# Optimization experiments

Measured on AMD Instinct MI355X. Metric: run time of the kernel, lower is better.

Reference implementation:

```python
import jax, jax.numpy as jnp
import numpy as np

N_OPS = 8  # eset_ops_3_to_3: identity, 3 single-axis sums, 3 pair sums, full sum (broadcast back)


def _conv(x, w, b):
    # x: (N,C,H,W), w: (O,C,kh,kw), VALID conv, stride 1
    y = jax.lax.conv_general_dilated(x, w, (1, 1), 'VALID',
                                     dimension_numbers=('NCHW', 'OIHW', 'NCHW'))
    return y + b[None, :, None, None]


def _maxpool2(x):
    return jax.lax.reduce_window(x, -jnp.inf, jax.lax.max,
                                 (1, 1, 2, 2), (1, 1, 2, 2), 'VALID')


def _eq3to3(x, W, b):
    # x: (B,i,j,k,d) channels-last; W: (N_OPS,d,o); b: (o,)
    # Fused form: contract each summed basis op with its weight BEFORE broadcasting.
    si = x.sum(1)          # (B,j,k,d)
    sj = x.sum(2)          # (B,i,k,d)
    sk = x.sum(3)          # (B,i,j,d)
    sij = x.sum((1, 2))    # (B,k,d)
    sik = x.sum((1, 3))    # (B,j,d)
    sjk = x.sum((2, 3))    # (B,i,d)
    s = x.sum((1, 2, 3))   # (B,d)
    y = jnp.einsum('bijkd,do->bijko', x, W[0])
    y = y + jnp.einsum('bjkd,do->bjko', si, W[1])[:, None]
    y = y + jnp.einsum('bikd,do->biko', sj, W[2])[:, :, None]
    y = y + jnp.einsum('bijd,do->bijo', sk, W[3])[:, :, :, None]
    y = y + jnp.einsum('bkd,do->bko', sij, W[4])[:, None, None]
    y = y + jnp.einsum('bjd,do->bjo', sik, W[5])[:, None, :, None]
    y = y + jnp.einsum('bid,do->bio', sjk, W[6])[:, :, None, None]
    y = y + jnp.einsum('bd,do->bo', s, W[7])[:, None, None, None]
    return y + b


def setup_inputs() -> dict:
    key = jax.random.key(0)
    ks = jax.random.split(key, 14)
    B, k, h, w = 16, 40, 28, 28
    hid, out_dim = 64, 32
    flat = 64 * 4 * 4  # after conv5-pool2-conv5-pool2 on 28x28
    p = lambda ki, shape, fan: jax.random.normal(ki, shape, jnp.float32) / np.sqrt(fan)
    return {
        'x': jax.random.normal(ks[0], (B, k, h, w), jnp.float32),
        'conv1_w': p(ks[1], (32, 1, 5, 5), 25),
        'conv1_b': jnp.zeros((32,), jnp.float32),
        'conv2_w': p(ks[2], (64, 32, 5, 5), 32 * 25),
        'conv2_b': jnp.zeros((64,), jnp.float32),
        'fc_w': p(ks[3], (flat, hid), flat),
        'fc_b': jnp.zeros((hid,), jnp.float32),
        'eq1_w': p(ks[4], (N_OPS, hid, hid), N_OPS * hid) * 0.1,
        'eq1_b': jnp.zeros((hid,), jnp.float32),
        'eq2_w': p(ks[5], (N_OPS, hid, out_dim), N_OPS * hid) * 0.1,
        'eq2_b': jnp.zeros((out_dim,), jnp.float32),
        'out_w': p(ks[6], (out_dim, 1), out_dim),
        'out_b': jnp.zeros((1,), jnp.float32),
    }


def reference(x, conv1_w, conv1_b, conv2_w, conv2_b, fc_w, fc_b,
              eq1_w, eq1_b, eq2_w, eq2_b, out_w, out_b):
    B, k, h, w = x.shape
    z = x.reshape(B * k, 1, h, w)
    z = _maxpool2(jax.nn.relu(_conv(z, conv1_w, conv1_b)))
    z = _maxpool2(jax.nn.relu(_conv(z, conv2_w, conv2_b)))
    z = z.reshape(B * k, -1) @ fc_w + fc_b
    e = jax.nn.relu(z).reshape(B, k, -1)          # (B,k,d)
    t = jnp.einsum('bid,bjd,bkd->bijkd', e, e, e)  # (B,k,k,k,d) cubic tensor
    y = jax.nn.relu(_eq3to3(t, eq1_w, eq1_b))
    y = _eq3to3(y, eq2_w, eq2_b)                   # (B,k,k,k,out_dim)
    y = jax.nn.relu(y).sum(axis=(1, 2, 3))         # (B,out_dim); dropout_prob=0 (eval)
    y = jax.nn.relu(y)
    return y @ out_w + out_b                       # (B,1)
```

## Files before the change

kernel.cpp:

```cpp
#include <hip/hip_runtime.h>
#include <hip/hip_bf16.h>


typedef unsigned short u16;
typedef __attribute__((ext_vector_type(8))) short bf8_t;
typedef __attribute__((ext_vector_type(4))) float f4_t;

#define LSTR 72

__device__ inline u16 f2bf(float f){
  union { float f; unsigned u; } v; v.f = f;
  unsigned r = v.u + 0x7fffu + ((v.u >> 16) & 1u);
  return (u16)(r >> 16);
}
__device__ inline float bflo(unsigned u){ union { unsigned x; float f; } v; v.x = u << 16; return v.f; }
__device__ inline float bfhi(unsigned u){ union { unsigned x; float f; } v; v.x = u & 0xffff0000u; return v.f; }
__device__ inline unsigned pack2(float a, float b){ return (unsigned)f2bf(a) | ((unsigned)f2bf(b) << 16); }
__device__ inline unsigned permpack(float lo, float hi){
  union { float f; unsigned u; } x, y; x.f = lo; y.f = hi;
  return __builtin_amdgcn_perm(y.u, x.u, 0x07060302u);
}
__device__ inline void unpack8(bf8_t x, float* o){
  union { bf8_t v; unsigned u[4]; } q; q.v = x;
  #pragma unroll
  for (int p = 0; p < 4; ++p){ o[2*p] = bflo(q.u[p]); o[2*p+1] = bfhi(q.u[p]); }
}

__global__ __launch_bounds__(256) void kwp(const float* __restrict__ w2, const float* __restrict__ fcw,
                                           u16* __restrict__ wt2, u16* __restrict__ fcwT){
  int tid = blockIdx.x*256 + threadIdx.x, stride = gridDim.x*256;
  for (int i = tid; i < 51200; i += stride){
    int tap = i >> 11, rc = i & 2047, co = rc >> 5, ci = rc & 31;
    wt2[i] = f2bf(w2[co*800 + ci*25 + tap]);
  }
  for (int i = tid; i < 65536; i += stride){
    int o = i >> 10, k = i & 1023;
    fcwT[i] = f2bf(fcw[k*64 + o]);
  }
}

__global__ __launch_bounds__(256) void kconv1(const float* __restrict__ x, const float* __restrict__ w1,
                                              const float* __restrict__ b1, u16* __restrict__ z1t){
  __shared__ float simg[784];
  int img = blockIdx.x, tid = threadIdx.x;
  for (int i = tid; i < 784; i += 256) simg[i] = x[img*784 + i];
  const int c = tid & 31;
  float wc[25];
  #pragma unroll
  for (int t = 0; t < 25; ++t) wc[t] = w1[c*25 + t];
  const float bb = b1[c];
  __syncthreads();
  #pragma unroll 2
  for (int it = 0; it < 18; ++it){
    int p = (tid >> 5) + it*8;
    int py = p / 12, px = p % 12;
    float patch[36];
    const float* sp = &simg[2*py*28 + 2*px];
    #pragma unroll
    for (int yy = 0; yy < 6; ++yy)
      #pragma unroll
      for (int xx = 0; xx < 6; ++xx) patch[yy*6+xx] = sp[yy*28+xx];
    float mx = -1e30f;
    #pragma unroll
    for (int sy = 0; sy < 2; ++sy)
    #pragma unroll
    for (int sx = 0; sx < 2; ++sx){
      float s = bb;
      #pragma unroll
      for (int dy = 0; dy < 5; ++dy)
        #pragma unroll
        for (int dx = 0; dx < 5; ++dx)
          s += patch[(sy+dy)*6 + sx+dx] * wc[dy*5+dx];
      mx = fmaxf(mx, s);
    }
    z1t[(size_t)img*4608 + p*32 + c] = f2bf(fmaxf(mx, 0.f));
  }
}

__global__ __launch_bounds__(256) void kconv2m(const u16* __restrict__ z1t, const u16* __restrict__ wt2,
                                               const float* __restrict__ b2, u16* __restrict__ z2g){
  __shared__ __align__(16) u16 sz[4608];
  __shared__ __align__(16) u16 sz2[1024];
  int img = blockIdx.x, tid = threadIdx.x;
  for (int i = tid; i < 576; i += 256)
    ((uint4*)sz)[i] = ((const uint4*)(z1t + (size_t)img*4608))[i];
  __syncthreads();
  const int wave = tid >> 6, lane = tid & 63, l15 = lane & 15, quad = lane >> 4;
  const int y = wave*2 + (l15 >> 3), x = l15 & 7;
  f4_t acc[4];
  acc[0] = (f4_t){0.f,0.f,0.f,0.f}; acc[1] = acc[0]; acc[2] = acc[0]; acc[3] = acc[0];
  #pragma unroll
  for (int dy = 0; dy < 5; ++dy)
    #pragma unroll
    for (int dx = 0; dx < 5; ++dx){
      const int tap = dy*5 + dx;
      bf8_t af = *(const bf8_t*)&sz[((y+dy)*12 + (x+dx))*32 + quad*8];
      const u16* wp = wt2 + tap*2048 + l15*32 + quad*8;
      #pragma unroll
      for (int nt = 0; nt < 4; ++nt){
        bf8_t bf = *(const bf8_t*)(wp + nt*512);
        acc[nt] = __builtin_amdgcn_mfma_f32_16x16x32_bf16(af, bf, acc[nt], 0, 0, 0);
      }
    }
  #pragma unroll
  for (int nt = 0; nt < 4; ++nt){
    int co = nt*16 + l15;
    float v0 = fmaxf(acc[nt][0], acc[nt][1]);
    float v1 = fmaxf(acc[nt][2], acc[nt][3]);
    v0 = fmaxf(v0, __shfl_xor(v0, 32));
    v1 = fmaxf(v1, __shfl_xor(v1, 32));
    if (quad < 2){
      float bb = b2[co];
      sz2[co*16 + wave*4 + quad*2 + 0] = f2bf(fmaxf(v0 + bb, 0.f));
      sz2[co*16 + wave*4 + quad*2 + 1] = f2bf(fmaxf(v1 + bb, 0.f));
    }
  }
  __syncthreads();
  if (tid < 128) ((uint4*)(z2g + (size_t)img*1024))[tid] = ((const uint4*)sz2)[tid];
}

__global__ __launch_bounds__(256) void kfc(const u16* __restrict__ z2g, const u16* __restrict__ fcwT,
                                           const float* __restrict__ fcb,
                                           float* __restrict__ e_f, u16* __restrict__ e_b){
  __shared__ __align__(16) u16 sA[16*1032];
  int img0 = blockIdx.x*16, tid = threadIdx.x;
  for (int i = tid; i < 2048; i += 256){
    int row = i >> 7, c16 = i & 127;
    ((uint4*)(sA + row*1032))[c16] = ((const uint4*)(z2g + (size_t)(img0+row)*1024))[c16];
  }
  __syncthreads();
  const int wave = tid >> 6, lane = tid & 63, l15 = lane & 15, quad = lane >> 4;
  const int o = wave*16 + l15;
  f4_t acc = (f4_t){0.f,0.f,0.f,0.f};
  #pragma unroll 8
  for (int ks = 0; ks < 32; ++ks){
    bf8_t af = *(const bf8_t*)&sA[l15*1032 + ks*32 + quad*8];
    bf8_t bf = *(const bf8_t*)(fcwT + (size_t)o*1024 + ks*32 + quad*8);
    acc = __builtin_amdgcn_mfma_f32_16x16x32_bf16(af, bf, acc, 0, 0, 0);
  }
  const float bb = fcb[o];
  #pragma unroll
  for (int r = 0; r < 4; ++r){
    int img = img0 + quad*4 + r;
    float v = fmaxf(acc[r] + bb, 0.f);
    e_f[img*64 + o] = v;
    e_b[img*64 + o] = f2bf(v);
  }
}

__global__ __launch_bounds__(256) void kprep(const float* __restrict__ e_f, const float* __restrict__ e1w,
    const float* __restrict__ e1b, const float* __restrict__ e2w,
    float* __restrict__ Sg, u16* __restrict__ Vt, float* __restrict__ c0,
    float* __restrict__ P5, float* __restrict__ P6, u16* __restrict__ W2T0,
    u16* __restrict__ W3St){
  int b = blockIdx.x, ph = blockIdx.y, tid = threadIdx.x;
  __shared__ float se[2560];
  __shared__ float S[64], S2[64], S3[64];
  for (int i = tid; i < 2560; i += 256) se[i] = e_f[b*2560 + i];
  __syncthreads();
  if (tid < 64){
    float s = 0.f;
    for (int i = 0; i < 40; ++i) s += se[i*64 + tid];
    S[tid] = s; S2[tid] = s*s; S3[tid] = s*s*s;
    if (ph == 0) Sg[b*64 + tid] = s;
  }
  __syncthreads();
  {
    const int m = ph;
    for (int idx = tid; idx < 4096; idx += 256){
      int o = idx >> 6, d = idx & 63;
      float v;
      if (m == 0)      v = e1w[d*64 + o];
      else if (m == 1) v = S[d] * e1w[4096  + d*64 + o];
      else if (m == 2) v = S[d] * e1w[8192  + d*64 + o];
      else             v = S2[d] * e1w[16384 + d*64 + o];
      Vt[(size_t)b*16384 + m*4096 + idx] = f2bf(v);
    }
  }
  if (ph == 0){
    if (tid < 64){
      float a = e1b[tid];
      for (int d = 0; d < 64; ++d) a += S3[d] * e1w[7*4096 + d*64 + tid];
      c0[b*64 + tid] = a;
    }
  } else if (ph == 1){
    for (int idx = tid; idx < 4096; idx += 256){
      int o = idx >> 6, d = idx & 63;
      W3St[(size_t)b*4096 + idx] = f2bf(S[d] * e1w[3*4096 + d*64 + o]);
    }
  } else {
    int lo = (ph == 2) ? 0 : 1280, hi = lo + 1280;
    for (int idx = lo + tid; idx < hi; idx += 256){
      int j = idx >> 6, o = idx & 63;
      float a5 = 0.f, a6 = 0.f;
      for (int d = 0; d < 64; ++d){
        float es = se[j*64 + d] * S2[d];
        a5 += es * e1w[5*4096 + d*64 + o];
        a6 += es * e1w[6*4096 + d*64 + o];
      }
      P5[(b*40+j)*64 + o] = a5;
      P6[(b*40+j)*64 + o] = a6;
    }
    if (ph == 3 && b == 0){
      for (int idx = tid; idx < 2048; idx += 256){
        int o = idx >> 6, d = idx & 63;
        W2T0[o*64 + d] = f2bf(e2w[d*32 + o]);
      }
    }
  }
}

__global__ __launch_bounds__(256) void kpq(const u16* __restrict__ e_b, const u16* __restrict__ W3St,
    const float* __restrict__ P5, const float* __restrict__ P6, const float* __restrict__ c0,
    float* __restrict__ Q3c){
  __shared__ __align__(16) u16 sP[48*LSTR];
  __shared__ __align__(16) u16 sW[64*LSTR];
  int blk = blockIdx.x, b = blk/40, i = blk%40, tid = threadIdx.x;
  const int wave = tid >> 6, lane = tid & 63, l15 = lane & 15, quad = lane >> 4;
  for (int idx = tid; idx < 2048; idx += 256){
    int o = idx >> 5, c = idx & 31;
    ((unsigned*)(sW + o*LSTR))[c] = ((const unsigned*)(W3St + (size_t)b*4096))[idx];
  }
  const unsigned* eb32 = (const unsigned*)(e_b + (size_t)b*2560);
  const unsigned* el = eb32 + i*32;
  #pragma unroll
  for (int it = 0; it < 6; ++it){
    int idx = tid + it*256;
    int k = idx >> 5, d2 = idx & 31;
    unsigned pv = 0;
    if (k < 40){
      unsigned ul = el[d2], uk = eb32[k*32 + d2];
      pv = pack2(bflo(ul)*bflo(uk), bfhi(ul)*bfhi(uk));
    }
    ((unsigned*)(sP + k*LSTR))[d2] = pv;
  }
  __syncthreads();
  bf8_t wf[2];
  #pragma unroll
  for (int ks = 0; ks < 2; ++ks)
    wf[ks] = *(const bf8_t*)&sW[(wave*16 + l15)*LSTR + ks*32 + quad*8];
  f4_t acc[3];
  #pragma unroll
  for (int n = 0; n < 3; ++n){
    f4_t a = (f4_t){0.f,0.f,0.f,0.f};
    #pragma unroll
    for (int ks = 0; ks < 2; ++ks){
      bf8_t pkf = *(const bf8_t*)&sP[(n*16 + l15)*LSTR + ks*32 + quad*8];
      a = __builtin_amdgcn_mfma_f32_16x16x32_bf16(wf[ks], pkf, a, 0, 0, 0);
    }
    acc[n] = a;
  }
  const int obase = wave*16 + quad*4;
  f4_t p6v = *(const f4_t*)&P6[(b*40+i)*64 + obase];
  f4_t c0v = *(const f4_t*)&c0[b*64 + obase];
  #pragma unroll
  for (int n = 0; n < 3; ++n){
    int j = n*16 + l15;
    if (j < 40){
      f4_t p5v = *(const f4_t*)&P5[(b*40+j)*64 + obase];
      f4_t outv;
      #pragma unroll
      for (int r = 0; r < 4; ++r) outv[r] = acc[n][r] + p5v[r] + p6v[r] + c0v[r];
      *(f4_t*)&Q3c[((size_t)((b*40+i)*40 + j))*64 + obase] = outv;
    }
  }
}

__global__ __launch_bounds__(256, 4) void kh01(
    const u16* __restrict__ e_b, const float* __restrict__ e_f,
    const u16* __restrict__ Vt, const float* __restrict__ Q3c,
    float* __restrict__ si2, float* __restrict__ sj2, float* __restrict__ sk2)
{
  __shared__ __align__(16) u16 sU[48*LSTR];
  __shared__ __align__(16) u16 sB1[64*LSTR];
  __shared__ __align__(16) u16 sB0[64*LSTR];
  __shared__ __align__(16) float sUf[2560];
  const int tid = threadIdx.x;
  const int b = blockIdx.x / 40, fix = blockIdx.x % 40;
  const int mode = blockIdx.y;
  const int wave = tid >> 6, lane = tid & 63, l15 = lane & 15, quad = lane >> 4;

  for (int idx = tid; idx < 1536; idx += 256){
    int r = idx >> 5, c = idx & 31;
    unsigned v = (r < 40) ? ((const unsigned*)e_b)[(b*40 + r)*32 + c] : 0u;
    ((unsigned*)(sU + r*LSTR))[c] = v;
  }
  for (int i = tid; i < 2560; i += 256) sUf[i] = e_f[b*2560 + i];
  const unsigned* eg = (const unsigned*)(e_b + (size_t)(b*40 + fix)*64);
  const unsigned* Vb = (const unsigned*)(Vt + (size_t)b*16384);
  for (int idx = tid; idx < 2048; idx += 256){
    int o = idx >> 5, d2 = idx & 31;
    unsigned eu = eg[d2];
    unsigned v0 = Vb[o*32 + d2];
    unsigned vA = Vb[(2-mode)*2048 + o*32 + d2];
    unsigned vB = Vb[(1+mode)*2048 + o*32 + d2];
    unsigned v3 = Vb[3*2048 + o*32 + d2];
    float e0 = bflo(eu), e1 = bfhi(eu);
    ((unsigned*)(sB1 + o*LSTR))[d2] = pack2(e0*bflo(v0)+bflo(vA), e1*bfhi(v0)+bfhi(vA));
    ((unsigned*)(sB0 + o*LSTR))[d2] = pack2(e0*bflo(vB)+bflo(v3), e1*bfhi(vB)+bfhi(v3));
  }
  __syncthreads();

  float b1uf[2][8];
  bf8_t ua[3][2];
  f4_t Y0[3];
  {
    bf8_t b0f[2], b1f[2];
    #pragma unroll
    for (int ks = 0; ks < 2; ++ks){
      b1f[ks] = *(const bf8_t*)&sB1[(wave*16 + l15)*LSTR + ks*32 + quad*8];
      b0f[ks] = *(const bf8_t*)&sB0[(wave*16 + l15)*LSTR + ks*32 + quad*8];
      unpack8(b1f[ks], b1uf[ks]);
    }
    #pragma unroll
    for (int n = 0; n < 3; ++n){
      f4_t a = (f4_t){0.f,0.f,0.f,0.f};
      #pragma unroll
      for (int ks = 0; ks < 2; ++ks){
        ua[n][ks] = *(const bf8_t*)&sU[(n*16 + l15)*LSTR + ks*32 + quad*8];
        a = __builtin_amdgcn_mfma_f32_16x16x32_bf16(b0f[ks], ua[n][ks], a, 0, 0, 0);
      }
      Y0[n] = a;
    }
  }

  const int obase = wave*16 + quad*4;
  f4_t sacc[3];
  sacc[0] = (f4_t){0.f,0.f,0.f,0.f}; sacc[1] = sacc[0]; sacc[2] = sacc[0];

  for (int l = 0; l < 40; ++l){
    const int qidx = mode ? (fix*40 + l) : (l*40 + fix);
    f4_t cadd = *(const f4_t*)&Q3c[((size_t)(b*1600 + qidx))*64 + obase];
    const float* ep = &sUf[l*64 + quad*8];
    f4_t ea = *(const f4_t*)(ep);
    f4_t eb = *(const f4_t*)(ep + 4);
    f4_t ec = *(const f4_t*)(ep + 32);
    f4_t ed = *(const f4_t*)(ep + 36);
    union { bf8_t v; unsigned u[4]; } m0, m1;
    m0.u[0] = permpack(b1uf[0][0]*ea[0], b1uf[0][1]*ea[1]);
    m0.u[1] = permpack(b1uf[0][2]*ea[2], b1uf[0][3]*ea[3]);
    m0.u[2] = permpack(b1uf[0][4]*eb[0], b1uf[0][5]*eb[1]);
    m0.u[3] = permpack(b1uf[0][6]*eb[2], b1uf[0][7]*eb[3]);
    m1.u[0] = permpack(b1uf[1][0]*ec[0], b1uf[1][1]*ec[1]);
    m1.u[1] = permpack(b1uf[1][2]*ec[2], b1uf[1][3]*ec[3]);
    m1.u[2] = permpack(b1uf[1][4]*ed[0], b1uf[1][5]*ed[1]);
    m1.u[3] = permpack(b1uf[1][6]*ed[2], b1uf[1][7]*ed[3]);
    f4_t khs = (f4_t){0.f,0.f,0.f,0.f};
    #pragma unroll
    for (int n = 0; n < 3; ++n){
      f4_t a = Y0[n];
      a = __builtin_amdgcn_mfma_f32_16x16x32_bf16(m0.v, ua[n][0], a, 0, 0, 0);
      a = __builtin_amdgcn_mfma_f32_16x16x32_bf16(m1.v, ua[n][1], a, 0, 0, 0);
      const bool valid = (n < 2) | (l15 < 8);
      #pragma unroll
      for (int r = 0; r < 4; ++r){
        float h = fmaxf(a[r] + cadd[r], 0.f);
        h = valid ? h : 0.f;
        sacc[n][r] += h;
        khs[r] += h;
      }
    }
    if (mode == 0){
      #pragma unroll
      for (int r = 0; r < 4; ++r){
        float v = khs[r];
        v += __shfl_xor(v, 1); v += __shfl_xor(v, 2);
        v += __shfl_xor(v, 4); v += __shfl_xor(v, 8);
        khs[r] = v;
      }
      if (l15 == 0)
        *(f4_t*)&sk2[((size_t)((b*40 + l)*40 + fix))*64 + obase] = khs;
    }
  }
  float* dst = mode ? sj2 : si2;
  #pragma unroll
  for (int n = 0; n < 3; ++n){
    int k = n*16 + l15;
    if (k < 40)
      *(f4_t*)&dst[((size_t)((b*40 + fix)*40 + k))*64 + obase] = sacc[n];
  }
}

__global__ __launch_bounds__(256) void k5a(const float* __restrict__ si2, const float* __restrict__ sj2,
    const float* __restrict__ e2w, const float* __restrict__ e2b,
    float* __restrict__ A4, float* __restrict__ A5, float* __restrict__ A6, float* __restrict__ A7){
  int b = blockIdx.x, half = blockIdx.y, tid = threadIdx.x;
  __shared__ float ssij[2560], ssik[2560], ssjk[2560], ss2[64];
  if (half == 0){
    for (int idx = tid; idx < 2560; idx += 256){
      int k = idx >> 6, d = idx & 63;
      float a = 0.f;
      for (int j = 0; j < 40; ++j) a += si2[((size_t)(b*40+j)*40 + k)*64 + d];
      ssij[idx] = a;
    }
  } else {
    for (int idx = tid; idx < 2560; idx += 256){
      int j = idx >> 6, d = idx & 63;
      float a = 0.f, c = 0.f;
      const float* p = &si2[(size_t)(b*40+j)*2560 + d];
      const float* q = &sj2[(size_t)(b*40+j)*2560 + d];
      for (int k = 0; k < 40; ++k){ a += p[k*64]; c += q[k*64]; }
      ssik[idx] = a;
      ssjk[idx] = c;
    }
  }
  __syncthreads();
  if (half == 0 && tid < 64){
    float a = 0.f;
    for (int k = 0; k < 40; ++k) a += ssij[k*64 + tid];
    ss2[tid] = a;
  }
  __syncthreads();
  if (half == 0){
    for (int idx = tid; idx < 1280; idx += 256){
      int k = idx >> 5, o = idx & 31;
      float a4 = 0.f;
      for (int d = 0; d < 64; ++d) a4 += ssij[k*64+d] * e2w[4*2048 + d*32 + o];
      A4[(b*40+k)*32 + o] = a4;
    }
    if (tid < 32){
      float a = e2b[tid];
      for (int d = 0; d < 64; ++d) a += ss2[d] * e2w[7*2048 + d*32 + tid];
      A7[b*32 + tid] = a;
    }
  } else {
    for (int idx = tid; idx < 1280; idx += 256){
      int k = idx >> 5, o = idx & 31;
      float a5 = 0.f, a6 = 0.f;
      for (int d = 0; d < 64; ++d){
        a5 += ssik[k*64+d] * e2w[5*2048 + d*32 + o];
        a6 += ssjk[k*64+d] * e2w[6*2048 + d*32 + o];
      }
      A5[(b*40+k)*32 + o] = a5;
      A6[(b*40+k)*32 + o] = a6;
    }
  }
}

__global__ __launch_bounds__(256) void k5b(const float* __restrict__ si2, const float* __restrict__ sj2,
    const float* __restrict__ sk2, const float* __restrict__ e2w,
    const float* __restrict__ A4, const float* __restrict__ A5, const float* __restrict__ A6,
    const float* __restrict__ A7,
    float* __restrict__ A1p, float* __restrict__ A2t, float* __restrict__ Cc){
  int which = blockIdx.y;
  int blk = blockIdx.x, b = blk/40, f = blk%40, tid = threadIdx.x;
  __shared__ float src[2560];
  __shared__ float wt[32*65];
  const float* S = (which == 0) ? si2 : (which == 1) ? sj2 : sk2;
  int wop = which + 1;
  for (int idx = tid; idx < 2560; idx += 256) src[idx] = S[(size_t)(b*40+f)*2560 + idx];
  for (int idx = tid; idx < 2048; idx += 256){
    int o = idx >> 6, d = idx & 63;
    wt[o*65 + d] = e2w[wop*2048 + d*32 + o];
  }
  __syncthreads();
  for (int idx = tid; idx < 1280; idx += 256){
    int r = idx >> 5, o = idx & 31;
    float a = 0.f;
    for (int d = 0; d < 64; ++d) a += src[r*64 + d] * wt[o*65 + d];
    size_t oi = ((size_t)(b*40+f)*40 + r)*32 + o;
    if (which == 0)      A1p[oi] = a + A4[(b*40+r)*32 + o];
    else if (which == 1) A2t[oi] = a;
    else                 Cc[oi]  = a + A5[(b*40+r)*32 + o] + A6[(b*40+f)*32 + o] + A7[b*32 + o];
  }
}

__global__ __launch_bounds__(256, 3) void kh2(
    const u16* __restrict__ e_b, const float* __restrict__ e_f,
    const u16* __restrict__ Vt, const float* __restrict__ Q3c, const u16* __restrict__ W2T0,
    const float* __restrict__ A1p, const float* __restrict__ A2t, const float* __restrict__ Cc,
    float* __restrict__ out_part)
{
  __shared__ __align__(16) u16 sU[48*LSTR];
  __shared__ __align__(16) u16 sBB[2][64*LSTR];
  __shared__ __align__(16) u16 sW2[32*LSTR];
  __shared__ __align__(16) float sUf[2560];
  __shared__ float soacc[32];
  u16* sB1 = sBB[0];
  u16* sB0 = sBB[1];
  const int tid = threadIdx.x;
  const int b = blockIdx.x / 40, fix = blockIdx.x % 40;
  const int wave = tid >> 6, lane = tid & 63, l15 = lane & 15, quad = lane >> 4;

  for (int idx = tid; idx < 1536; idx += 256){
    int r = idx >> 5, c = idx & 31;
    unsigned v = (r < 40) ? ((const unsigned*)e_b)[(b*40 + r)*32 + c] : 0u;
    ((unsigned*)(sU + r*LSTR))[c] = v;
  }
  for (int i = tid; i < 2560; i += 256) sUf[i] = e_f[b*2560 + i];
  const unsigned* eg = (const unsigned*)(e_b + (size_t)(b*40 + fix)*64);
  const unsigned* Vb = (const unsigned*)(Vt + (size_t)b*16384);
  for (int idx = tid; idx < 2048; idx += 256){
    int o = idx >> 5, d2 = idx & 31;
    unsigned eu = eg[d2];
    unsigned v0 = Vb[o*32 + d2];
    unsigned vA = Vb[2*2048 + o*32 + d2];
    unsigned vB = Vb[1*2048 + o*32 + d2];
    unsigned v3 = Vb[3*2048 + o*32 + d2];
    float e0 = bflo(eu), e1 = bfhi(eu);
    ((unsigned*)(sB1 + o*LSTR))[d2] = pack2(e0*bflo(v0)+bflo(vA), e1*bfhi(v0)+bfhi(vA));
    ((unsigned*)(sB0 + o*LSTR))[d2] = pack2(e0*bflo(vB)+bflo(v3), e1*bfhi(vB)+bfhi(v3));
  }
  for (int idx = tid; idx < 1024; idx += 256){
    int o = idx >> 5, c = idx & 31;
    ((unsigned*)(sW2 + o*LSTR))[c] = ((const unsigned*)W2T0)[idx];
  }
  if (tid < 32) soacc[tid] = 0.f;
  __syncthreads();

  float b1uf[2][8];
  bf8_t ua[3][2], wfA[2][2];
  f4_t Y0[3];
  {
    bf8_t b0f[2], b1f[2];
    #pragma unroll
    for (int ks = 0; ks < 2; ++ks){
      b1f[ks] = *(const bf8_t*)&sB1[(wave*16 + l15)*LSTR + ks*32 + quad*8];
      b0f[ks] = *(const bf8_t*)&sB0[(wave*16 + l15)*LSTR + ks*32 + quad*8];
      unpack8(b1f[ks], b1uf[ks]);
      #pragma unroll
      for (int m = 0; m < 2; ++m)
        wfA[m][ks] = *(const bf8_t*)&sW2[(m*16 + l15)*LSTR + ks*32 + quad*8];
    }
    #pragma unroll
    for (int n = 0; n < 3; ++n){
      f4_t a = (f4_t){0.f,0.f,0.f,0.f};
      #pragma unroll
      for (int ks = 0; ks < 2; ++ks){
        ua[n][ks] = *(const bf8_t*)&sU[(n*16 + l15)*LSTR + ks*32 + quad*8];
        a = __builtin_amdgcn_mfma_f32_16x16x32_bf16(b0f[ks], ua[n][ks], a, 0, 0, 0);
      }
      Y0[n] = a;
    }
  }
  __syncthreads();

  const int obase = wave*16 + quad*4;
  const int o2b   = quad*4;
  const int kme   = wave*16 + l15;
  const int kmc   = kme < 40 ? kme : 39;
  const bool kval = (kme < 40) & (wave < 3);
  f4_t pa1[2], psum[2];
  psum[0] = (f4_t){0.f,0.f,0.f,0.f}; psum[1] = psum[0];
  if (wave < 3){
    #pragma unroll
    for (int m = 0; m < 2; ++m)
      pa1[m] = *(const f4_t*)&A1p[((size_t)((b*40 + fix)*40 + kmc))*32 + m*16 + o2b];
  }

  for (int l = 0; l < 40; ++l){
    f4_t a2v[2], ccv[2];
    if (wave < 3){
      #pragma unroll
      for (int m = 0; m < 2; ++m){
        a2v[m] = *(const f4_t*)&A2t[((size_t)((b*40 + l)*40 + kmc))*32 + m*16 + o2b];
        ccv[m] = *(const f4_t*)&Cc [((size_t)((b*40 + l)*40 + fix))*32 + m*16 + o2b];
      }
    }
    f4_t cadd = *(const f4_t*)&Q3c[((size_t)(b*1600 + l*40 + fix))*64 + obase];
    const float* ep = &sUf[l*64 + quad*8];
    f4_t ea = *(const f4_t*)(ep);
    f4_t eb = *(const f4_t*)(ep + 4);
    f4_t ec = *(const f4_t*)(ep + 32);
    f4_t ed = *(const f4_t*)(ep + 36);
    union { bf8_t v; unsigned u[4]; } m0, m1;
    m0.u[0] = permpack(b1uf[0][0]*ea[0], b1uf[0][1]*ea[1]);
    m0.u[1] = permpack(b1uf[0][2]*ea[2], b1uf[0][3]*ea[3]);
    m0.u[2] = permpack(b1uf[0][4]*eb[0], b1uf[0][5]*eb[1]);
    m0.u[3] = permpack(b1uf[0][6]*eb[2], b1uf[0][7]*eb[3]);
    m1.u[0] = permpack(b1uf[1][0]*ec[0], b1uf[1][1]*ec[1]);
    m1.u[1] = permpack(b1uf[1][2]*ec[2], b1uf[1][3]*ec[3]);
    m1.u[2] = permpack(b1uf[1][4]*ed[0], b1uf[1][5]*ed[1]);
    m1.u[3] = permpack(b1uf[1][6]*ed[2], b1uf[1][7]*ed[3]);
    u16* Hb = sBB[l & 1];
    #pragma unroll
    for (int n = 0; n < 3; ++n){
      f4_t a = Y0[n];
      a = __builtin_amdgcn_mfma_f32_16x16x32_bf16(m0.v, ua[n][0], a, 0, 0, 0);
      a = __builtin_amdgcn_mfma_f32_16x16x32_bf16(m1.v, ua[n][1], a, 0, 0, 0);
      const bool valid = (n < 2) | (l15 < 8);
      unsigned p0 = 0, p1 = 0;
      if (valid){
        p0 = pack2(fmaxf(a[0] + cadd[0], 0.f), fmaxf(a[1] + cadd[1], 0.f));
        p1 = pack2(fmaxf(a[2] + cadd[2], 0.f), fmaxf(a[3] + cadd[3], 0.f));
      }
      uint2 pw; pw.x = p0; pw.y = p1;
      *(uint2*)&Hb[(n*16 + l15)*LSTR + obase] = pw;
    }
    __syncthreads();
    if (wave < 3){
      bf8_t hB[2];
      #pragma unroll
      for (int ks = 0; ks < 2; ++ks)
        hB[ks] = *(const bf8_t*)&Hb[(wave*16 + l15)*LSTR + ks*32 + quad*8];
      #pragma unroll
      for (int m = 0; m < 2; ++m){
        f4_t y = (f4_t){0.f,0.f,0.f,0.f};
        y = __builtin_amdgcn_mfma_f32_16x16x32_bf16(wfA[m][0], hB[0], y, 0, 0, 0);
        y = __builtin_amdgcn_mfma_f32_16x16x32_bf16(wfA[m][1], hB[1], y, 0, 0, 0);
        if (kval){
          #pragma unroll
          for (int r = 0; r < 4; ++r){
            float v = y[r] + pa1[m][r] + a2v[m][r] + ccv[m][r];
            psum[m][r] += v > 0.f ? v : 0.f;
          }
        }
      }
    }
  }

  if (wave < 3){
    #pragma unroll
    for (int m = 0; m < 2; ++m)
      #pragma unroll
      for (int r = 0; r < 4; ++r){
        float v = psum[m][r];
        v += __shfl_xor(v, 1); v += __shfl_xor(v, 2);
        v += __shfl_xor(v, 4); v += __shfl_xor(v, 8);
        if (l15 == 0) atomicAdd(&soacc[m*16 + o2b + r], v);
      }
  }
  __syncthreads();
  if (tid < 32) out_part[(b*40 + fix)*32 + tid] = soacc[tid];
}

__global__ __launch_bounds__(64) void k7(const float* __restrict__ out_part, const float* __restrict__ ow,
                                         const float* __restrict__ ob, float* __restrict__ out){
  int b = threadIdx.x;
  if (b < 16){
    float res = ob[0];
    for (int o = 0; o < 32; ++o){
      float s = 0.f;
      for (int j = 0; j < 40; ++j) s += out_part[(b*40+j)*32 + o];
      s = s > 0.f ? s : 0.f;
      res += s * ow[o];
    }
    out[b] = res;
  }
}

extern "C" void kernel_launch(void* const* d_in, const int* in_sizes, int n_in,
                              void* d_out, int out_size, void* d_ws, size_t ws_size,
                              hipStream_t stream){
  const float* x    = (const float*)d_in[0];
  const float* c1w  = (const float*)d_in[1];
  const float* c1b  = (const float*)d_in[2];
  const float* c2w  = (const float*)d_in[3];
  const float* c2b  = (const float*)d_in[4];
  const float* fcw  = (const float*)d_in[5];
  const float* fcb  = (const float*)d_in[6];
  const float* e1w  = (const float*)d_in[7];
  const float* e1b  = (const float*)d_in[8];
  const float* e2w  = (const float*)d_in[9];
  const float* e2b  = (const float*)d_in[10];
  const float* ow   = (const float*)d_in[11];
  const float* ob   = (const float*)d_in[12];

  char* ws = (char*)d_ws;
  size_t off = 0;
  auto alloc = [&](size_t bytes) -> void* {
    void* p = ws + off;
    off += (bytes + 255) & ~(size_t)255;
    return p;
  };
  u16*   z1t  = (u16*)  alloc((size_t)640*4608*2);
  u16*   wt2  = (u16*)  alloc(51200*2);
  u16*   fcwT = (u16*)  alloc(65536*2);
  u16*   z2g  = (u16*)  alloc((size_t)640*1024*2);
  float* e_f  = (float*)alloc(40960*4);
  u16*   e_b  = (u16*)  alloc(40960*2);
  float* Sg   = (float*)alloc(1024*4);
  u16*   Vt   = (u16*)  alloc((size_t)16*16384*2);
  float* c0   = (float*)alloc(1024*4);
  float* P5   = (float*)alloc(40960*4);
  float* P6   = (float*)alloc(40960*4);
  u16*   W2T0 = (u16*)  alloc(2048*2);
  u16*   W3St = (u16*)  alloc((size_t)16*4096*2);
  float* Q3c  = (float*)alloc((size_t)1638400*4);
  float* si2  = (float*)alloc((size_t)1638400*4);
  float* sj2  = (float*)alloc((size_t)1638400*4);
  float* sk2  = (float*)alloc((size_t)1638400*4);
  float* A4   = (float*)alloc(20480*4);
  float* A5   = (float*)alloc(20480*4);
  float* A6   = (float*)alloc(20480*4);
  float* A7   = (float*)alloc(512*4);
  float* A1p  = (float*)alloc((size_t)819200*4);
  float* A2t  = (float*)alloc((size_t)819200*4);
  float* Cc   = (float*)alloc((size_t)819200*4);
  float* op   = (float*)alloc(20480*4);
  (void)in_sizes; (void)n_in; (void)out_size; (void)ws_size;

  kwp    <<<32,  256, 0, stream>>>(c2w, fcw, wt2, fcwT);
  kconv1 <<<640, 256, 0, stream>>>(x, c1w, c1b, z1t);
  kconv2m<<<640, 256, 0, stream>>>(z1t, wt2, c2b, z2g);
  kfc    <<<40,  256, 0, stream>>>(z2g, fcwT, fcb, e_f, e_b);
  kprep  <<<dim3(16,4), 256, 0, stream>>>(e_f, e1w, e1b, e2w, Sg, Vt, c0, P5, P6, W2T0, W3St);
  kpq    <<<640, 256, 0, stream>>>(e_b, W3St, P5, P6, c0, Q3c);
  kh01   <<<dim3(640,2), 256, 0, stream>>>(e_b, e_f, Vt, Q3c, si2, sj2, sk2);
  k5a    <<<dim3(16,2), 256, 0, stream>>>(si2, sj2, e2w, e2b, A4, A5, A6, A7);
  k5b    <<<dim3(640,3), 256, 0, stream>>>(si2, sj2, sk2, e2w, A4, A5, A6, A7, A1p, A2t, Cc);
  kh2    <<<640, 256, 0, stream>>>(e_b, e_f, Vt, Q3c, W2T0, A1p, A2t, Cc, op);
  k7     <<<1, 64, 0, stream>>>(op, ow, ob, (float*)d_out);
}
```

Before: 329.6 us.

## Alias shared memory in kh01/kh2, prefetch Q3c, vectorize k5b, parallelize k7

kh01 and kh2 now overlay the float e_f staging buffer on the bf16 buffers in one shared array, staging e_f through registers and writing it only after the bf16 buffers are consumed. The aim is less LDS per block and therefore more resident blocks. kh01 also loads the next step's Q3c values one iteration ahead to hide global latency. k5b switches to float4 shared tiles with register accumulation over 5 rows per thread, and k7 spreads the final reduction over 512 threads with shuffles. The extra barriers and the register staging add sync overhead and register pressure.

```diff
diff --git a/kernel.cpp b/kernel.cpp
--- a/kernel.cpp
+++ b/kernel.cpp
@@ -271,10 +271,11 @@
     const u16* __restrict__ Vt, const float* __restrict__ Q3c,
     float* __restrict__ si2, float* __restrict__ sj2, float* __restrict__ sk2)
 {
-  __shared__ __align__(16) u16 sU[48*LSTR];
-  __shared__ __align__(16) u16 sB1[64*LSTR];
-  __shared__ __align__(16) u16 sB0[64*LSTR];
-  __shared__ __align__(16) float sUf[2560];
+  __shared__ __align__(16) char smem[25344];
+  u16*   sU  = (u16*)smem;
+  u16*   sB1 = (u16*)(smem + 6912);
+  u16*   sB0 = (u16*)(smem + 16128);
+  float* sUf = (float*)smem;
   const int tid = threadIdx.x;
   const int b = blockIdx.x / 40, fix = blockIdx.x % 40;
   const int mode = blockIdx.y;
@@ -285,7 +286,9 @@
     unsigned v = (r < 40) ? ((const unsigned*)e_b)[(b*40 + r)*32 + c] : 0u;
     ((unsigned*)(sU + r*LSTR))[c] = v;
   }
-  for (int i = tid; i < 2560; i += 256) sUf[i] = e_f[b*2560 + i];
+  float efr[10];
+  #pragma unroll
+  for (int t = 0; t < 10; ++t) efr[t] = e_f[b*2560 + tid + t*256];
   const unsigned* eg = (const unsigned*)(e_b + (size_t)(b*40 + fix)*64);
   const unsigned* Vb = (const unsigned*)(Vt + (size_t)b*16384);
   for (int idx = tid; idx < 2048; idx += 256){
@@ -323,14 +326,23 @@
       Y0[n] = a;
     }
   }
+  __syncthreads();
+  #pragma unroll
+  for (int t = 0; t < 10; ++t) sUf[tid + t*256] = efr[t];
+  __syncthreads();
 
   const int obase = wave*16 + quad*4;
   f4_t sacc[3];
   sacc[0] = (f4_t){0.f,0.f,0.f,0.f}; sacc[1] = sacc[0]; sacc[2] = sacc[0];
 
+  auto qaddr = [&](int l) -> const f4_t* {
+    int qidx = mode ? (fix*40 + l) : (l*40 + fix);
+    return (const f4_t*)&Q3c[((size_t)(b*1600 + qidx))*64 + obase];
+  };
+  f4_t cadd_n = *qaddr(0);
   for (int l = 0; l < 40; ++l){
-    const int qidx = mode ? (fix*40 + l) : (l*40 + fix);
-    f4_t cadd = *(const f4_t*)&Q3c[((size_t)(b*1600 + qidx))*64 + obase];
+    f4_t cadd = cadd_n;
+    if (l < 39) cadd_n = *qaddr(l + 1);
     const float* ep = &sUf[l*64 + quad*8];
     f4_t ea = *(const f4_t*)(ep);
     f4_t eb = *(const f4_t*)(ep + 4);
@@ -444,21 +456,36 @@
     float* __restrict__ A1p, float* __restrict__ A2t, float* __restrict__ Cc){
   int which = blockIdx.y;
   int blk = blockIdx.x, b = blk/40, f = blk%40, tid = threadIdx.x;
-  __shared__ float src[2560];
-  __shared__ float wt[32*65];
+  __shared__ __align__(16) f4_t ssrc[640];
+  __shared__ __align__(16) f4_t swt[32*17];
   const float* S = (which == 0) ? si2 : (which == 1) ? sj2 : sk2;
   int wop = which + 1;
-  for (int idx = tid; idx < 2560; idx += 256) src[idx] = S[(size_t)(b*40+f)*2560 + idx];
-  for (int idx = tid; idx < 2048; idx += 256){
-    int o = idx >> 6, d = idx & 63;
-    wt[o*65 + d] = e2w[wop*2048 + d*32 + o];
-  }
-  __syncthreads();
-  for (int idx = tid; idx < 1280; idx += 256){
-    int r = idx >> 5, o = idx & 31;
-    float a = 0.f;
-    for (int d = 0; d < 64; ++d) a += src[r*64 + d] * wt[o*65 + d];
+  const f4_t* Sg4 = (const f4_t*)&S[(size_t)(b*40+f)*2560];
+  for (int idx = tid; idx < 640; idx += 256) ssrc[idx] = Sg4[idx];
+  for (int idx = tid; idx < 512; idx += 256){
+    int o = idx >> 4, d4 = idx & 15;
+    f4_t w;
+    #pragma unroll
+    for (int r = 0; r < 4; ++r) w[r] = e2w[wop*2048 + (4*d4+r)*32 + o];
+    swt[o*17 + d4] = w;
+  }
+  __syncthreads();
+  const int o = tid & 31, rb = tid >> 5;
+  float acc[5] = {0.f, 0.f, 0.f, 0.f, 0.f};
+  #pragma unroll 4
+  for (int d4 = 0; d4 < 16; ++d4){
+    f4_t w = swt[o*17 + d4];
+    #pragma unroll
+    for (int it = 0; it < 5; ++it){
+      f4_t s = ssrc[(rb + 8*it)*16 + d4];
+      acc[it] += s[0]*w[0] + s[1]*w[1] + s[2]*w[2] + s[3]*w[3];
+    }
+  }
+  #pragma unroll
+  for (int it = 0; it < 5; ++it){
+    int r = rb + 8*it;
     size_t oi = ((size_t)(b*40+f)*40 + r)*32 + o;
+    float a = acc[it];
     if (which == 0)      A1p[oi] = a + A4[(b*40+r)*32 + o];
     else if (which == 1) A2t[oi] = a;
     else                 Cc[oi]  = a + A5[(b*40+r)*32 + o] + A6[(b*40+f)*32 + o] + A7[b*32 + o];
@@ -471,13 +498,13 @@
     const float* __restrict__ A1p, const float* __restrict__ A2t, const float* __restrict__ Cc,
     float* __restrict__ out_part)
 {
-  __shared__ __align__(16) u16 sU[48*LSTR];
-  __shared__ __align__(16) u16 sBB[2][64*LSTR];
-  __shared__ __align__(16) u16 sW2[32*LSTR];
-  __shared__ __align__(16) float sUf[2560];
-  __shared__ float soacc[32];
-  u16* sB1 = sBB[0];
-  u16* sB0 = sBB[1];
+  __shared__ __align__(16) char smem[30080];
+  u16*   sB1 = (u16*)smem;
+  u16*   sB0 = (u16*)(smem + 9216);
+  u16*   sU  = (u16*)(smem + 18432);
+  u16*   sW2 = (u16*)(smem + 18432 + 6912);
+  float* sUf = (float*)(smem + 18432);
+  float* soacc = (float*)(smem + 29952);
   const int tid = threadIdx.x;
   const int b = blockIdx.x / 40, fix = blockIdx.x % 40;
   const int wave = tid >> 6, lane = tid & 63, l15 = lane & 15, quad = lane >> 4;
@@ -487,7 +514,9 @@
     unsigned v = (r < 40) ? ((const unsigned*)e_b)[(b*40 + r)*32 + c] : 0u;
     ((unsigned*)(sU + r*LSTR))[c] = v;
   }
-  for (int i = tid; i < 2560; i += 256) sUf[i] = e_f[b*2560 + i];
+  float efr[10];
+  #pragma unroll
+  for (int t = 0; t < 10; ++t) efr[t] = e_f[b*2560 + tid + t*256];
   const unsigned* eg = (const unsigned*)(e_b + (size_t)(b*40 + fix)*64);
   const unsigned* Vb = (const unsigned*)(Vt + (size_t)b*16384);
   for (int idx = tid; idx < 2048; idx += 256){
@@ -533,6 +562,9 @@
       Y0[n] = a;
     }
   }
+  __syncthreads();
+  #pragma unroll
+  for (int t = 0; t < 10; ++t) sUf[tid + t*256] = efr[t];
   __syncthreads();
 
   const int obase = wave*16 + quad*4;
@@ -572,7 +604,7 @@
     m1.u[1] = permpack(b1uf[1][2]*ec[2], b1uf[1][3]*ec[3]);
     m1.u[2] = permpack(b1uf[1][4]*ed[0], b1uf[1][5]*ed[1]);
     m1.u[3] = permpack(b1uf[1][6]*ed[2], b1uf[1][7]*ed[3]);
-    u16* Hb = sBB[l & 1];
+    u16* Hb = (u16*)(smem + (l & 1)*9216);
     #pragma unroll
     for (int n = 0; n < 3; ++n){
       f4_t a = Y0[n];
@@ -624,19 +656,17 @@
   if (tid < 32) out_part[(b*40 + fix)*32 + tid] = soacc[tid];
 }
 
-__global__ __launch_bounds__(64) void k7(const float* __restrict__ out_part, const float* __restrict__ ow,
-                                         const float* __restrict__ ob, float* __restrict__ out){
-  int b = threadIdx.x;
-  if (b < 16){
-    float res = ob[0];
-    for (int o = 0; o < 32; ++o){
-      float s = 0.f;
-      for (int j = 0; j < 40; ++j) s += out_part[(b*40+j)*32 + o];
-      s = s > 0.f ? s : 0.f;
-      res += s * ow[o];
-    }
-    out[b] = res;
-  }
+__global__ __launch_bounds__(512) void k7(const float* __restrict__ out_part, const float* __restrict__ ow,
+                                          const float* __restrict__ ob, float* __restrict__ out){
+  int tid = threadIdx.x;
+  int b = tid >> 5, o = tid & 31;
+  float s = 0.f;
+  for (int j = 0; j < 40; ++j) s += out_part[(b*40 + j)*32 + o];
+  s = s > 0.f ? s : 0.f;
+  float v = s * ow[o];
+  v += __shfl_xor(v, 1); v += __shfl_xor(v, 2); v += __shfl_xor(v, 4);
+  v += __shfl_xor(v, 8); v += __shfl_xor(v, 16);
+  if (o == 0) out[b] = v + ob[0];
 }
 
 extern "C" void kernel_launch(void* const* d_in, const int* in_sizes, int n_in,
@@ -700,5 +730,5 @@
   k5a    <<<dim3(16,2), 256, 0, stream>>>(si2, sj2, e2w, e2b, A4, A5, A6, A7);
   k5b    <<<dim3(640,3), 256, 0, stream>>>(si2, sj2, sk2, e2w, A4, A5, A6, A7, A1p, A2t, Cc);
   kh2    <<<640, 256, 0, stream>>>(e_b, e_f, Vt, Q3c, W2T0, A1p, A2t, Cc, op);
-  k7     <<<1, 64, 0, stream>>>(op, ow, ob, (float*)d_out);
-}
+  k7     <<<1, 512, 0, stream>>>(op, ow, ob, (float*)d_out);
+}
```

Measured after the change: 290.3 us. 11.9% less time.
